# Kernel optimization log

Measured on AMD Instinct MI355X. Metric: run time of the kernel, lower is better.

Reference implementation:

```python
import jax, jax.numpy as jnp
import numpy as np

N = 50000   # nodes
E = 600000  # edges (avg degree 12)
F = 16      # raw node features
P = 32      # n_channels_preproc
C = 128     # n_channels
L = 6       # n_gnn_layers
LBL = 2     # n_labels


def _dense_init(k, fan_in, shape):
    return (jax.random.normal(k, shape, jnp.float32) / np.float32(np.sqrt(fan_in)))


def setup_inputs() -> dict:
    key = jax.random.key(0)
    ks = jax.random.split(key, 12)
    return {
        "x": jax.random.normal(ks[0], (N, F), jnp.float32),
        "edge_src": jax.random.randint(ks[1], (E,), 0, N, dtype=jnp.int32),
        "edge_dst": jax.random.randint(ks[2], (E,), 0, N, dtype=jnp.int32),
        "edge_weight": jax.random.uniform(ks[3], (E,), jnp.float32),  # normalized-adjacency values
        "preproc_W": _dense_init(ks[4], F, (F, P)), "preproc_b": jnp.zeros((P,), jnp.float32),
        "fc_in1_W": _dense_init(ks[5], P, (P, C)), "fc_in1_b": jnp.zeros((C,), jnp.float32),
        "fc_in2_W": _dense_init(ks[6], P, (P, C)), "fc_in2_b": jnp.zeros((C,), jnp.float32),
        "gcn_W": _dense_init(ks[7], C, (L, C, C)), "gcn_b": jnp.zeros((L, C), jnp.float32),
        "fcg_W": _dense_init(ks[8], 2 * C, (L, 2 * C, C)), "fcg_b": jnp.zeros((L, C), jnp.float32),
        "last1_W": _dense_init(ks[9], 2 * C, (2 * C, C)), "last1_b": jnp.zeros((C,), jnp.float32),
        "last2_W": _dense_init(ks[10], C, (C, LBL)), "last2_b": jnp.zeros((LBL,), jnp.float32),
    }


def reference(x, edge_src, edge_dst, edge_weight,
              preproc_W, preproc_b, fc_in1_W, fc_in1_b, fc_in2_W, fc_in2_b,
              gcn_W, gcn_b, fcg_W, fcg_b, last1_W, last1_b, last2_W, last2_b):
    relu = jax.nn.relu
    h = relu(x @ preproc_W + preproc_b)                      # preproc Dense
    node_id = relu(h @ fc_in1_W + fc_in1_b)                  # node identity branch
    h = relu(h @ fc_in2_W + fc_in2_b)

    def layer(h, params):
        W, b, Wf, bf = params
        # GCNConv: act(A_hat @ (h @ W) + b), A_hat as COO edge list
        hw = h @ W                                           # [N, C]
        msg = hw[edge_src] * edge_weight[:, None]            # [E, C]
        agg = jax.ops.segment_sum(msg, edge_dst, num_segments=N)
        g = relu(agg + b)
        merged = jnp.concatenate([node_id, g], axis=-1)      # [N, 2C]
        return relu(merged @ Wf + bf), None                  # dropout = identity (eval)

    h, _ = jax.lax.scan(layer, h, (gcn_W, gcn_b, fcg_W, fcg_b))

    merged = jnp.concatenate([node_id, h], axis=-1)
    h = relu(merged @ last1_W + last1_b)
    return jax.nn.sigmoid(h @ last2_W + last2_b)             # [N, n_labels]
```

## Files before the change

### kernel.cpp

```cpp
#include <hip/hip_runtime.h>
#include <cstddef>
#include <cstdint>

#define NN 50000
#define NE 600000
#define NB 391

typedef __attribute__((ext_vector_type(8))) short bf16x8;
typedef __attribute__((ext_vector_type(4))) float f32x4;

#define SWZ(x) (((x) ^ ((x) >> 2)) & 3)

__device__ __forceinline__ float bf2f(ushort u) {
    return __uint_as_float(((uint32_t)u) << 16);
}
__device__ __forceinline__ ushort f2bf(float f) {
    uint32_t b = __float_as_uint(f);
    return (ushort)((b + 0x7FFF + ((b >> 16) & 1)) >> 16);
}

__global__ __launch_bounds__(256)
void convbh_kernel(const float* __restrict__ f1W, const float* __restrict__ f2W,
                   const float* __restrict__ gW, const float* __restrict__ fgW,
                   const float* __restrict__ l1W, ushort* __restrict__ wt,
                   const int* __restrict__ dst, int* __restrict__ bcnt)
{
    if (blockIdx.x < 1312) {
        int i = blockIdx.x * 256 + threadIdx.x;
        if (i >= 335872) return;
        float v;
        if (i < 4096) {
            int c = i >> 5, k = i & 31;
            v = f1W[k * 128 + c];
        } else if (i < 8192) {
            int j = i - 4096; int c = j >> 5, k = j & 31;
            v = f2W[k * 128 + c];
        } else if (i < 8192 + 98304) {
            int j = i - 8192; int l = j >> 14, r = j & 16383;
            int c = r >> 7, k = r & 127;
            v = gW[l * 16384 + k * 128 + c];
        } else if (i < 8192 + 98304 + 196608) {
            int j = i - (8192 + 98304); int l = j >> 15, r = j & 32767;
            int c = r >> 8, k = r & 255;
            v = fgW[l * 32768 + k * 128 + c];
        } else {
            int j = i - (8192 + 98304 + 196608);
            int c = j >> 8, k = j & 255;
            v = l1W[k * 128 + c];
        }
        wt[i] = f2bf(v);
    } else {
        __shared__ int h[NB];
        int tx = threadIdx.x;
        for (int i = tx; i < NB; i += 256) h[i] = 0;
        __syncthreads();
        int e0 = (blockIdx.x - 1312) * 1024;
#pragma unroll
        for (int k = 0; k < 4; ++k) {
            int e = e0 + k * 256 + tx;
            if (e < NE) atomicAdd(&h[dst[e] >> 7], 1);
        }
        __syncthreads();
        for (int i = tx; i < NB; i += 256)
            if (h[i]) atomicAdd(&bcnt[i], h[i]);
    }
}

__global__ __launch_bounds__(512)
void bscan_kernel(const int* __restrict__ bcnt, int* __restrict__ bbase,
                  int* __restrict__ bcur)
{
    __shared__ int buf[512];
    int t = threadIdx.x;
    int v = (t < NB) ? bcnt[t] : 0;
    buf[t] = v;
    __syncthreads();
    for (int s = 1; s < 512; s <<= 1) {
        int u = (t >= s) ? buf[t - s] : 0;
        __syncthreads();
        buf[t] += u;
        __syncthreads();
    }
    if (t < NB) {
        int ex = buf[t] - v;
        bbase[t] = ex;
        bcur[t]  = ex;
    }
    if (t == 0) bbase[NB] = NE;
}

__global__ __launch_bounds__(256)
void pass1_kernel(const int* __restrict__ src, const int* __restrict__ dst,
                  const float* __restrict__ w, int* __restrict__ bcur,
                  unsigned int* __restrict__ stage_pk,
// ... 61 lines not shown
        int node0 = b * 128;
        if (tx < 128) {
            int n = node0 + tx;
            if (n < NN) off[n] = base + lofs[tx];
            h[tx] = 0;
        }
        if (b == NB - 1 && tx == 0) off[NN] = NE;
        __syncthreads();
        for (int i = tx; i < cnt; i += 256) {
            int d = stage_dl[base + i];
            int r = atomicAdd(&h[d], 1);
            esw[base + lofs[d] + r] = stage_pk[base + i];
        }
    } else {
        __shared__ float Wl[512];
        __shared__ float bl[32];
        int tx = threadIdx.x;
        Wl[tx]       = preW[tx];
        Wl[tx + 256] = preW[tx + 256];
        if (tx < 32) bl[tx] = preb[tx];
        __syncthreads();
        int n = (blockIdx.x - NB) * 256 + tx;
        if (n >= NN) return;
        float xr[16];
        const float4* xp = (const float4*)(x + (size_t)n * 16);
#pragma unroll
        for (int q = 0; q < 4; ++q) {
            float4 v = xp[q];
            xr[q*4+0]=v.x; xr[q*4+1]=v.y; xr[q*4+2]=v.z; xr[q*4+3]=v.w;
        }
        float acc[32];
#pragma unroll
        for (int c = 0; c < 32; ++c) acc[c] = bl[c];
#pragma unroll
        for (int k = 0; k < 16; ++k)
#pragma unroll
            for (int c = 0; c < 32; ++c)
                acc[c] = fmaf(xr[k], Wl[k*32+c], acc[c]);
        ushort4* op = (ushort4*)(h0b + (size_t)n * 32);
#pragma unroll
        for (int q = 0; q < 8; ++q) {
            ushort4 v;
            v.x = f2bf(fmaxf(acc[q*4+0], 0.f));
            v.y = f2bf(fmaxf(acc[q*4+1], 0.f));
            v.z = f2bf(fmaxf(acc[q*4+2], 0.f));
            v.w = f2bf(fmaxf(acc[q*4+3], 0.f));
            op[q] = v;
        }
    }
}

__global__ __launch_bounds__(128)
void fc1f0_kernel(const ushort* __restrict__ h0b,
                  const ushort* __restrict__ wf1, const float* __restrict__ f1b,
                  ushort* __restrict__ nidb,
                  const ushort* __restrict__ wf2, const float* __restrict__ f2b,
                  const ushort* __restrict__ wg, ushort* __restrict__ hwb)
{
    __shared__ ushort Atile[64 * 32];
    __shared__ ushort Btile[128 * 32];
    __shared__ ushort Xt[64 * 128];
    const int tx   = threadIdx.x;
    const int wave = tx >> 6;
    const int lane = tx & 63;
    const int rs  = lane >> 2;
    const int chn = (lane & 3) ^ SWZ(rs);
    const int m    = lane & 15;
    const int quad = lane >> 4;
    const int slot = quad ^ SWZ(m);

    if (blockIdx.x < 782) {
        const int bm = blockIdx.x * 64;
        f32x4 acc0[8], acc1[8];
#pragma unroll
        for (int t = 0; t < 8; ++t) {
            acc0[t] = (f32x4){0.f, 0.f, 0.f, 0.f};
            acc1[t] = (f32x4){0.f, 0.f, 0.f, 0.f};
        }
#pragma unroll
        for (int i = 0; i < 2; ++i) {
            int seg = wave + 2 * i;
            int row = seg * 16 + rs;
            int ar  = bm + row; if (ar >= NN) ar = NN - 1;
            __builtin_amdgcn_global_load_lds(
                (const __attribute__((address_space(1))) void*)
                    (h0b + (size_t)ar * 32 + chn * 8),
                (__attribute__((address_space(3))) void*)(Atile + seg * 512),
                16, 0, 0);
        }
#pragma unroll
        for (int i = 0; i < 4; ++i) {
            int seg = wave + 2 * i;
            int col = seg * 16 + rs;
            __builtin_amdgcn_global_load_lds(
                (const __attribute__((address_space(1))) void*)
                    (wf1 + (size_t)col * 32 + chn * 8),
                (__attribute__((address_space(3))) void*)(Btile + seg * 512),
                16, 0, 0);
        }
        __syncthreads();
        bf16x8 af0 = *(const bf16x8*)(Atile + (wave * 32 + m) * 32 + slot * 8);
        bf16x8 af1 = *(const bf16x8*)(Atile + (wave * 32 + 16 + m) * 32 + slot * 8);
#pragma unroll
        for (int t = 0; t < 8; ++t) {
            bf16x8 bfr = *(const bf16x8*)(Btile + (t * 16 + m) * 32 + slot * 8);
            acc0[t] = __builtin_amdgcn_mfma_f32_16x16x32_bf16(af0, bfr, acc0[t], 0, 0, 0);
            acc1[t] = __builtin_amdgcn_mfma_f32_16x16x32_bf16(af1, bfr, acc1[t], 0, 0, 0);
        }
        __syncthreads();
#pragma unroll
        for (int half = 0; half < 2; ++half) {
            const int orow0 = bm + wave * 32 + half * 16 + quad * 4;
#pragma unroll
            for (int t = 0; t < 8; ++t) {
                int col = t * 16 + m;
                float bb = f1b[col];
                f32x4 a = half ? acc1[t] : acc0[t];
#pragma unroll
                for (int r = 0; r < 4; ++r) {
                    int row = orow0 + r;
                    if (row < NN)
                        nidb[(size_t)row * 128 + col] = f2bf(fmaxf(a[r] + bb, 0.f));
                }
            }
        }
    } else {
        const int bm = (blockIdx.x - 782) * 64;
        f32x4 acc0[8], acc1[8];
#pragma unroll
        for (int t = 0; t < 8; ++t) {
            acc0[t] = (f32x4){0.f, 0.f, 0.f, 0.f};
            acc1[t] = (f32x4){0.f, 0.f, 0.f, 0.f};
        }
#pragma unroll
        for (int i = 0; i < 2; ++i) {
            int seg = wave + 2 * i;
            int row = seg * 16 + rs;
            int ar  = bm + row; if (ar >= NN) ar = NN - 1;
            __builtin_amdgcn_global_load_lds(
                (const __attribute__((address_space(1))) void*)
                    (h0b + (size_t)ar * 32 + chn * 8),
                (__attribute__((address_space(3))) void*)(Atile + seg * 512),
                16, 0, 0);
        }
#pragma unroll
        for (int i = 0; i < 4; ++i) {
            int seg = wave + 2 * i;
            int col = seg * 16 + rs;
            __builtin_amdgcn_global_load_lds(
                (const __attribute__((address_space(1))) void*)
                    (wf2 + (size_t)col * 32 + chn * 8),
                (__attribute__((address_space(3))) void*)(Btile + seg * 512),
                16, 0, 0);
        }
        __syncthreads();
        {
            bf16x8 af0 = *(const bf16x8*)(Atile + (wave * 32 + m) * 32 + slot * 8);
            bf16x8 af1 = *(const bf16x8*)(Atile + (wave * 32 + 16 + m) * 32 + slot * 8);
#pragma unroll
            for (int t = 0; t < 8; ++t) {
                bf16x8 bfr = *(const bf16x8*)(Btile + (t * 16 + m) * 32 + slot * 8);
                acc0[t] = __builtin_amdgcn_mfma_f32_16x16x32_bf16(af0, bfr, acc0[t], 0, 0, 0);
                acc1[t] = __builtin_amdgcn_mfma_f32_16x16x32_bf16(af1, bfr, acc1[t], 0, 0, 0);
            }
        }
        __syncthreads();
#pragma unroll
        for (int half = 0; half < 2; ++half) {
            int rbase = wave * 32 + half * 16 + quad * 4;
#pragma unroll
            for (int t = 0; t < 8; ++t) {
                int col = t * 16 + m;
                float bb = f2b[col];
                int c32 = col >> 5, within = col & 7, ks = (col >> 3) & 3;
                f32x4 a = half ? acc1[t] : acc0[t];
#pragma unroll
                for (int r = 0; r < 4; ++r) {
                    int row = rbase + r;
                    int pos = ks ^ SWZ(row & 15);
                    Xt[row * 128 + c32 * 32 + pos * 8 + within] =
                        f2bf(fmaxf(a[r] + bb, 0.f));
                }
            }
        }
#pragma unroll
        for (int t = 0; t < 8; ++t) {
            acc0[t] = (f32x4){0.f, 0.f, 0.f, 0.f};
            acc1[t] = (f32x4){0.f, 0.f, 0.f, 0.f};
        }
        __syncthreads();
        for (int c32 = 0; c32 < 4; ++c32) {
            int kk = c32 * 32;
#pragma unroll
            for (int i = 0; i < 4; ++i) {
                int seg = wave + 2 * i;
                int col = seg * 16 + rs;
                __builtin_amdgcn_global_load_lds(
                    (const __attribute__((address_space(1))) void*)
                        (wg + (size_t)col * 128 + kk + chn * 8),
                    (__attribute__((address_space(3))) void*)(Btile + seg * 512),
                    16, 0, 0);
            }
            __syncthreads();
            bf16x8 af0 = *(const bf16x8*)(Xt + (wave * 32 + m) * 128 + kk + slot * 8);
            bf16x8 af1 = *(const bf16x8*)(Xt + (wave * 32 + 16 + m) * 128 + kk + slot * 8);
#pragma unroll
            for (int t = 0; t < 8; ++t) {
                bf16x8 bfr = *(const bf16x8*)(Btile + (t * 16 + m) * 32 + slot * 8);
                acc0[t] = __builtin_amdgcn_mfma_f32_16x16x32_bf16(af0, bfr, acc0[t], 0, 0, 0);
                acc1[t] = __builtin_amdgcn_mfma_f32_16x16x32_bf16(af1, bfr, acc1[t], 0, 0, 0);
            }
            __syncthreads();
        }
#pragma unroll
        for (int half = 0; half < 2; ++half) {
            const int orow0 = bm + wave * 32 + half * 16 + quad * 4;
#pragma unroll
            for (int t = 0; t < 8; ++t) {
                int col = t * 16 + m;
                f32x4 a = half ? acc1[t] : acc0[t];
#pragma unroll
                for (int r = 0; r < 4; ++r) {
                    int row = orow0 + r;
                    if (row < NN)
                        hwb[(size_t)row * 128 + col] = f2bf(a[r]);
                }
            }
        }
    }
}

__global__ __launch_bounds__(128)
void gemm_fused(const ushort* __restrict__ A1, int K1,
                const ushort* __restrict__ A2, int K2,
                const ushort* __restrict__ Wt, const float* __restrict__ bias,
                const ushort* __restrict__ Wg,
                ushort* __restrict__ out_hw, int nrows)
{
    __shared__ ushort Atile[64 * 32];
    __shared__ ushort Btile[128 * 32];
    __shared__ ushort Xt[64 * 128];
    const int tx   = threadIdx.x;
    const int wave = tx >> 6;
    const int lane = tx & 63;
    const int bm   = blockIdx.x * 64;
    const int Ktot = K1 + K2;

    const int rs  = lane >> 2;
    const int chn = (lane & 3) ^ SWZ(rs);
    const int m    = lane & 15;
    const int quad = lane >> 4;
    const int slot = quad ^ SWZ(m);

    f32x4 acc0[8], acc1[8];
#pragma unroll
    for (int t = 0; t < 8; ++t) {
        acc0[t] = (f32x4){0.f, 0.f, 0.f, 0.f};
        acc1[t] = (f32x4){0.f, 0.f, 0.f, 0.f};
    }

    for (int kk = 0; kk < Ktot; kk += 32) {
        const ushort* asrc; int astr, kl;
        if (kk < K1) { asrc = A1; astr = K1; kl = kk; }
        else         { asrc = A2; astr = K2; kl = kk - K1; }
#pragma unroll
        for (int i = 0; i < 2; ++i) {
            int seg = wave + 2 * i;
            int row = seg * 16 + rs;
            int ar  = bm + row; if (ar >= nrows) ar = nrows - 1;
            __builtin_amdgcn_global_load_lds(
                (const __attribute__((address_space(1))) void*)
                    (asrc + (size_t)ar * astr + kl + chn * 8),
                (__attribute__((address_space(3))) void*)(Atile + seg * 512),
                16, 0, 0);
        }
#pragma unroll
        for (int i = 0; i < 4; ++i) {
            int seg = wave + 2 * i;
            int col = seg * 16 + rs;
            __builtin_amdgcn_global_load_lds(
                (const __attribute__((address_space(1))) void*)
                    (Wt + (size_t)col * Ktot + kk + chn * 8),
                (__attribute__((address_space(3))) void*)(Btile + seg * 512),
                16, 0, 0);
        }
        __syncthreads();
        bf16x8 af0 = *(const bf16x8*)(Atile + (wave * 32 + m) * 32 + slot * 8);
        bf16x8 af1 = *(const bf16x8*)(Atile + (wave * 32 + 16 + m) * 32 + slot * 8);
#pragma unroll
        for (int t = 0; t < 8; ++t) {
            bf16x8 bfr = *(const bf16x8*)(Btile + (t * 16 + m) * 32 + slot * 8);
            acc0[t] = __builtin_amdgcn_mfma_f32_16x16x32_bf16(af0, bfr, acc0[t], 0, 0, 0);
            acc1[t] = __builtin_amdgcn_mfma_f32_16x16x32_bf16(af1, bfr, acc1[t], 0, 0, 0);
        }
        __syncthreads();
    }

#pragma unroll
    for (int half = 0; half < 2; ++half) {
        int rbase = wave * 32 + half * 16 + quad * 4;
#pragma unroll
        for (int t = 0; t < 8; ++t) {
            int col = t * 16 + m;
            float bb = bias[col];
            int c32 = col >> 5, within = col & 7, ks = (col >> 3) & 3;
            f32x4 a = half ? acc1[t] : acc0[t];
#pragma unroll
            for (int r = 0; r < 4; ++r) {
                int row = rbase + r;
                int pos = ks ^ SWZ(row & 15);
                Xt[row * 128 + c32 * 32 + pos * 8 + within] =
                    f2bf(fmaxf(a[r] + bb, 0.f));
            }
        }
    }
#pragma unroll
    for (int t = 0; t < 8; ++t) {
        acc0[t] = (f32x4){0.f, 0.f, 0.f, 0.f};
        acc1[t] = (f32x4){0.f, 0.f, 0.f, 0.f};
    }
    __syncthreads();

    for (int c32 = 0; c32 < 4; ++c32) {
        int kk = c32 * 32;
#pragma unroll
        for (int i = 0; i < 4; ++i) {
            int seg = wave + 2 * i;
            int col = seg * 16 + rs;
            __builtin_amdgcn_global_load_lds(
                (const __attribute__((address_space(1))) void*)
                    (Wg + (size_t)col * 128 + kk + chn * 8),
                (__attribute__((address_space(3))) void*)(Btile + seg * 512),
                16, 0, 0);
        }
        __syncthreads();
        bf16x8 af0 = *(const bf16x8*)(Xt + (wave * 32 + m) * 128 + kk + slot * 8);
        bf16x8 af1 = *(const bf16x8*)(Xt + (wave * 32 + 16 + m) * 128 + kk + slot * 8);
#pragma unroll
        for (int t = 0; t < 8; ++t) {
            bf16x8 bfr = *(const bf16x8*)(Btile + (t * 16 + m) * 32 + slot * 8);
            acc0[t] = __builtin_amdgcn_mfma_f32_16x16x32_bf16(af0, bfr, acc0[t], 0, 0, 0);
            acc1[t] = __builtin_amdgcn_mfma_f32_16x16x32_bf16(af1, bfr, acc1[t], 0, 0, 0);
        }
        __syncthreads();
    }

#pragma unroll
    for (int half = 0; half < 2; ++half) {
        const int orow0 = bm + wave * 32 + half * 16 + quad * 4;
#pragma unroll
        for (int t = 0; t < 8; ++t) {
            int col = t * 16 + m;
            f32x4 a = half ? acc1[t] : acc0[t];
#pragma unroll
            for (int r = 0; r < 4; ++r) {
                int row = orow0 + r;
                if (row < nrows)
                    out_hw[(size_t)row * 128 + col] = f2bf(a[r]);
            }
        }
    }
}

__global__ __launch_bounds__(128)
void gemm_last(const ushort* __restrict__ nid, const ushort* __restrict__ agg,
               const ushort* __restrict__ Wt, const float* __restrict__ bias5,
               const ushort* __restrict__ Wl1, const float* __restrict__ l1b,
               const float* __restrict__ l2W, const float* __restrict__ l2b,
               float* __restrict__ out, int nrows)
{
    __shared__ ushort Atile[64 * 32];
    __shared__ ushort Btile[128 * 32];
    __shared__ ushort Xt[64 * 128];
    __shared__ float  w2s[256];
    const int tx   = threadIdx.x;
    const int wave = tx >> 6;
    const int lane = tx & 63;
    const int bm   = blockIdx.x * 64;

    w2s[tx]       = l2W[tx];
    w2s[tx + 128] = l2W[tx + 128];

    const int rs  = lane >> 2;
    const int chn = (lane & 3) ^ SWZ(rs);
    const int m    = lane & 15;
    const int quad = lane >> 4;
    const int slot = quad ^ SWZ(m);

    f32x4 acc0[8], acc1[8];
#pragma unroll
    for (int t = 0; t < 8; ++t) {
        acc0[t] = (f32x4){0.f, 0.f, 0.f, 0.f};
        acc1[t] = (f32x4){0.f, 0.f, 0.f, 0.f};
    }

    for (int kk = 0; kk < 256; kk += 32) {
        const ushort* asrc; int kl;
        if (kk < 128) { asrc = nid; kl = kk; }
        else          { asrc = agg; kl = kk - 128; }
#pragma unroll
        for (int i = 0; i < 2; ++i) {
            int seg = wave + 2 * i;
            int row = seg * 16 + rs;
            int ar  = bm + row; if (ar >= nrows) ar = nrows - 1;
            __builtin_amdgcn_global_load_lds(
                (const __attribute__((address_space(1))) void*)
                    (asrc + (size_t)ar * 128 + kl + chn * 8),
                (__attribute__((address_space(3))) void*)(Atile + seg * 512),
                16, 0, 0);
        }
#pragma unroll
        for (int i = 0; i < 4; ++i) {
            int seg = wave + 2 * i;
            int col = seg * 16 + rs;
            __builtin_amdgcn_global_load_lds(
                (const __attribute__((address_space(1))) void*)
                    (Wt + (size_t)col * 256 + kk + chn * 8),
                (__attribute__((address_space(3))) void*)(Btile + seg * 512),
                16, 0, 0);
        }
        __syncthreads();
        bf16x8 af0 = *(const bf16x8*)(Atile + (wave * 32 + m) * 32 + slot * 8);
        bf16x8 af1 = *(const bf16x8*)(Atile + (wave * 32 + 16 + m) * 32 + slot * 8);
#pragma unroll
        for (int t = 0; t < 8; ++t) {
            bf16x8 bfr = *(const bf16x8*)(Btile + (t * 16 + m) * 32 + slot * 8);
            acc0[t] = __builtin_amdgcn_mfma_f32_16x16x32_bf16(af0, bfr, acc0[t], 0, 0, 0);
            acc1[t] = __builtin_amdgcn_mfma_f32_16x16x32_bf16(af1, bfr, acc1[t], 0, 0, 0);
        }
        __syncthreads();
    }

#pragma unroll
    for (int half = 0; half < 2; ++half) {
        int rbase = wave * 32 + half * 16 + quad * 4;
#pragma unroll
        for (int t = 0; t < 8; ++t) {
            int col = t * 16 + m;
            float bb = bias5[col];
            int c32 = col >> 5, within = col & 7, ks = (col >> 3) & 3;
            f32x4 a = half ? acc1[t] : acc0[t];
#pragma unroll
            for (int r = 0; r < 4; ++r) {
                int row = rbase + r;
                int pos = ks ^ SWZ(row & 15);
                Xt[row * 128 + c32 * 32 + pos * 8 + within] =
                    f2bf(fmaxf(a[r] + bb, 0.f));
            }
        }
    }
#pragma unroll
    for (int t = 0; t < 8; ++t) {
        acc0[t] = (f32x4){0.f, 0.f, 0.f, 0.f};
        acc1[t] = (f32x4){0.f, 0.f, 0.f, 0.f};
    }
    __syncthreads();

    for (int c8 = 0; c8 < 8; ++c8) {
        int kk = c8 * 32;
        if (c8 < 4) {
#pragma unroll
            for (int i = 0; i < 2; ++i) {
                int seg = wave + 2 * i;
                int row = seg * 16 + rs;
                int ar  = bm + row; if (ar >= nrows) ar = nrows - 1;
                __builtin_amdgcn_global_load_lds(
                    (const __attribute__((address_space(1))) void*)
                        (nid + (size_t)ar * 128 + kk + chn * 8),
                    (__attribute__((address_space(3))) void*)(Atile + seg * 512),
                    16, 0, 0);
            }
        }
#pragma unroll
        for (int i = 0; i < 4; ++i) {
            int seg = wave + 2 * i;
            int col = seg * 16 + rs;
            __builtin_amdgcn_global_load_lds(
                (const __attribute__((address_space(1))) void*)
                    (Wl1 + (size_t)col * 256 + kk + chn * 8),
                (__attribute__((address_space(3))) void*)(Btile + seg * 512),
                16, 0, 0);
        }
        __syncthreads();
        bf16x8 af0, af1;
        if (c8 < 4) {
            af0 = *(const bf16x8*)(Atile + (wave * 32 + m) * 32 + slot * 8);
            af1 = *(const bf16x8*)(Atile + (wave * 32 + 16 + m) * 32 + slot * 8);
        } else {
            int ko = (c8 - 4) * 32;
            af0 = *(const bf16x8*)(Xt + (wave * 32 + m) * 128 + ko + slot * 8);
            af1 = *(const bf16x8*)(Xt + (wave * 32 + 16 + m) * 128 + ko + slot * 8);
        }
#pragma unroll
        for (int t = 0; t < 8; ++t) {
            bf16x8 bfr = *(const bf16x8*)(Btile + (t * 16 + m) * 32 + slot * 8);
            acc0[t] = __builtin_amdgcn_mfma_f32_16x16x32_bf16(af0, bfr, acc0[t], 0, 0, 0);
            acc1[t] = __builtin_amdgcn_mfma_f32_16x16x32_bf16(af1, bfr, acc1[t], 0, 0, 0);
        }
        __syncthreads();
    }

    float bb[8];
#pragma unroll
    for (int t = 0; t < 8; ++t) bb[t] = l1b[t * 16 + m];
    float b20 = l2b[0], b21 = l2b[1];
#pragma unroll
    for (int half = 0; half < 2; ++half) {
#pragma unroll
        for (int r = 0; r < 4; ++r) {
            float p0 = 0.f, p1 = 0.f;
#pragma unroll
            for (int t = 0; t < 8; ++t) {
                int col = t * 16 + m;
                f32x4 a = half ? acc1[t] : acc0[t];
                float v = fmaxf(a[r] + bb[t], 0.f);
                p0 = fmaf(v, w2s[col * 2 + 0], p0);
                p1 = fmaf(v, w2s[col * 2 + 1], p1);
            }
#pragma unroll
            for (int mask = 1; mask < 16; mask <<= 1) {
                p0 += __shfl_xor(p0, mask);
                p1 += __shfl_xor(p1, mask);
            }
            if (m == 0) {
                int row = bm + wave * 32 + half * 16 + quad * 4 + r;
                if (row < nrows) {
                    out[(size_t)row * 2 + 0] = 1.f / (1.f + __expf(-(p0 + b20)));
                    out[(size_t)row * 2 + 1] = 1.f / (1.f + __expf(-(p1 + b21)));
                }
            }
        }
    }
}

__global__ __launch_bounds__(256)
void gather_agg(const ushort* __restrict__ hw,
                const unsigned int* __restrict__ esw,
                const int* __restrict__ off, const float* __restrict__ gbias,
                ushort* __restrict__ agg)
{
    const int g    = blockIdx.x * 4 + (threadIdx.x >> 6);
    const int lane = threadIdx.x & 63;
    int n = g * 8;
    if (n >= NN) return;
    int n_end = n + 8; if (n_end > NN) n_end = NN;
    const int base = off[n];
    const int end  = off[n_end];
    int nb = off[n + 1];
    const ushort* hp = hw + lane * 2;
    const float g0 = gbias[lane * 2], g1 = gbias[lane * 2 + 1];
    float a0 = 0.f, a1 = 0.f;

    for (int chunk = base; chunk < end; chunk += 64) {
        int idx = chunk + lane;
        int pk = (idx < end) ? (int)esw[idx] : 0;
        int cnt = end - chunk; if (cnt > 64) cnt = 64;
        int cnt16 = (cnt + 15) & ~15;
        for (int j = 0; j < cnt16; j += 16) {
            int pp[16];
            unsigned int rv[16];
#pragma unroll
            for (int k = 0; k < 16; ++k)
                pp[k] = __builtin_amdgcn_readlane(pk, j + k);
#pragma unroll
            for (int k = 0; k < 16; ++k)
                rv[k] = *(const unsigned int*)(hp + (size_t)(pp[k] & 0x1FFFF) * 128);
#pragma unroll
            for (int k = 0; k < 16; ++k) {
                int e = chunk + j + k;
                while (e == nb) {
                    unsigned int o = (unsigned int)f2bf(fmaxf(a0 + g0, 0.f)) |
                                     ((unsigned int)f2bf(fmaxf(a1 + g1, 0.f)) << 16);
                    *(unsigned int*)(agg + (size_t)n * 128 + lane * 2) = o;
                    a0 = 0.f; a1 = 0.f;
                    ++n;
                    nb = (n < n_end) ? off[n + 1] : 0x7fffffff;
                }
                float w = bf2f((ushort)((unsigned int)pp[k] >> 17));
                a0 = fmaf(bf2f((ushort)(rv[k] & 0xffff)), w, a0);
                a1 = fmaf(bf2f((ushort)(rv[k] >> 16)),    w, a1);
            }
        }
    }
    while (n < n_end) {
        unsigned int o = (unsigned int)f2bf(fmaxf(a0 + g0, 0.f)) |
                         ((unsigned int)f2bf(fmaxf(a1 + g1, 0.f)) << 16);
        *(unsigned int*)(agg + (size_t)n * 128 + lane * 2) = o;
        a0 = 0.f; a1 = 0.f;
        ++n;
    }
}

extern "C" void kernel_launch(void* const* d_in, const int* in_sizes, int n_in,
                              void* d_out, int out_size, void* d_ws, size_t ws_size,
                              hipStream_t stream)
{
    const float* x    = (const float*)d_in[0];
    const int*   esrc = (const int*)  d_in[1];
    const int*   edst = (const int*)  d_in[2];
    const float* ew   = (const float*)d_in[3];
    const float* preW = (const float*)d_in[4];
    const float* preb = (const float*)d_in[5];
    const float* f1W  = (const float*)d_in[6];
    const float* f1b  = (const float*)d_in[7];
    const float* f2W  = (const float*)d_in[8];
    const float* f2b  = (const float*)d_in[9];
    const float* gW   = (const float*)d_in[10];
    const float* gb   = (const float*)d_in[11];
    const float* fgW  = (const float*)d_in[12];
    const float* fgb  = (const float*)d_in[13];
    const float* l1W  = (const float*)d_in[14];
    const float* l1b  = (const float*)d_in[15];
    const float* l2W  = (const float*)d_in[16];
    const float* l2b  = (const float*)d_in[17];
    float* out = (float*)d_out;

    ushort* wt   = (ushort*)d_ws;
    ushort* wf1  = wt;
    ushort* wf2  = wf1 + 4096;
    ushort* wg   = wf2 + 4096;
    ushort* wfg  = wg  + 98304;
    ushort* wl1  = wfg + 196608;
    ushort* h0b  = wl1 + 32768;
    ushort* nidb = h0b  + (size_t)NN * 32;
    ushort* hwb  = nidb + (size_t)NN * 128;
    ushort* aggb = hwb  + (size_t)NN * 128;
    ushort* endu = aggb + (size_t)NN * 128;
    unsigned int* esw      = (unsigned int*)(((uintptr_t)endu + 15) & ~(uintptr_t)15);
    unsigned int* stage_pk = esw + NE;
    int*          bcnt     = (int*)(stage_pk + NE);
    int*          bbase    = bcnt + NB + 1;
    int*          bcur     = bbase + NB + 1;
    int*          off      = bcur + NB + 1;
    unsigned char* stage_dl = (unsigned char*)(off + NN + 2);

    const int gblocks = (NN + 63) / 64;
    const int eblocks = (NE + 1023) / 1024;
    const int ngroups = (NN + 7) / 8;
    const int wblocks = (ngroups + 3) / 4;

    hipMemsetAsync(bcnt, 0, (size_t)NB * sizeof(int), stream);
    convbh_kernel<<<1312 + eblocks, 256, 0, stream>>>(f1W, f2W, gW, fgW, l1W, wt,
                                                      edst, bcnt);
    bscan_kernel<<<1, 512, 0, stream>>>(bcnt, bbase, bcur);
    pass1_kernel<<<eblocks, 256, 0, stream>>>(esrc, edst, ew, bcur, stage_pk, stage_dl);
    p2pre_kernel<<<NB + (NN + 255) / 256, 256, 0, stream>>>(stage_pk, stage_dl, bbase,
                                                            esw, off, x, preW, preb, h0b);

    fc1f0_kernel<<<2 * gblocks, 128, 0, stream>>>(h0b, wf1, f1b, nidb,
                                                  wf2, f2b, wg, hwb);
    for (int l = 0; l < 6; ++l) {
        gather_agg<<<wblocks, 256, 0, stream>>>(hwb, esw, off,
                                                gb + (size_t)l * 128, aggb);
        if (l < 5) {
            gemm_fused<<<gblocks, 128, 0, stream>>>(nidb, 128, aggb, 128,
                                                    wfg + (size_t)l * 32768,
                                                    fgb + (size_t)l * 128,
                                                    wg + (size_t)(l + 1) * 16384,
                                                    hwb, NN);
        }
    }
    gemm_last<<<gblocks, 128, 0, stream>>>(nidb, aggb,
                                           wfg + (size_t)5 * 32768,
                                           fgb + (size_t)5 * 128,
                                           wl1, l1b, l2W, l2b, out, NN);
}
```

Measured before the change: 420.4 us.

## Fuse edge gather-aggregation into per-layer GEMM kernels with ping-pong hw buffers

Removes the separate gather_agg kernel and performs the CSR gather/segment-sum for each 64-row tile directly inside the layer GEMM kernel. The aggregated rows are written into a swizzled LDS tile instead of a global agg buffer. Blocks grow to 4 waves with 16 rows each, and hw is double-buffered so one layer can read hw while the next layer's hw is written. This drops six kernel launches and the global write and re-read of the agg tensor. In exchange, LDS use per block rises and the gather and MFMA phases are serialized inside each block, which may reduce occupancy.

Measured after the change: 508.7 us. +21.0%, slower.

```diff
diff --git a/kernel.cpp b/kernel.cpp
--- a/kernel.cpp
+++ b/kernel.cpp
@@ -10,6 +10,11 @@
 typedef __attribute__((ext_vector_type(4))) float f32x4;
 
 #define SWZ(x) (((x) ^ ((x) >> 2)) & 3)
+
+#define GLDS16(src, dst)                                                     \
+    __builtin_amdgcn_global_load_lds(                                        \
+        (const __attribute__((address_space(1))) void*)(src),                \
+        (__attribute__((address_space(3))) void*)(dst), 16, 0, 0)
 
 __device__ __forceinline__ float bf2f(ushort u) {
     return __uint_as_float(((uint32_t)u) << 16);
@@ -237,21 +242,13 @@
             int seg = wave + 2 * i;
             int row = seg * 16 + rs;
             int ar  = bm + row; if (ar >= NN) ar = NN - 1;
-            __builtin_amdgcn_global_load_lds(
-                (const __attribute__((address_space(1))) void*)
-                    (h0b + (size_t)ar * 32 + chn * 8),
-                (__attribute__((address_space(3))) void*)(Atile + seg * 512),
-                16, 0, 0);
+            GLDS16(h0b + (size_t)ar * 32 + chn * 8, Atile + seg * 512);
         }
 #pragma unroll
         for (int i = 0; i < 4; ++i) {
             int seg = wave + 2 * i;
             int col = seg * 16 + rs;
-            __builtin_amdgcn_global_load_lds(
-                (const __attribute__((address_space(1))) void*)
-                    (wf1 + (size_t)col * 32 + chn * 8),
-                (__attribute__((address_space(3))) void*)(Btile + seg * 512),
-                16, 0, 0);
+            GLDS16(wf1 + (size_t)col * 32 + chn * 8, Btile + seg * 512);
         }
         __syncthreads();
         bf16x8 af0 = *(const bf16x8*)(Atile + (wave * 32 + m) * 32 + slot * 8);
@@ -292,21 +289,13 @@
             int seg = wave + 2 * i;
             int row = seg * 16 + rs;
             int ar  = bm + row; if (ar >= NN) ar = NN - 1;
-            __builtin_amdgcn_global_load_lds(
-                (const __attribute__((address_space(1))) void*)
-                    (h0b + (size_t)ar * 32 + chn * 8),
-                (__attribute__((address_space(3))) void*)(Atile + seg * 512),
-                16, 0, 0);
+            GLDS16(h0b + (size_t)ar * 32 + chn * 8, Atile + seg * 512);
         }
 #pragma unroll
         for (int i = 0; i < 4; ++i) {
             int seg = wave + 2 * i;
             int col = seg * 16 + rs;
-            __builtin_amdgcn_global_load_lds(
-                (const __attribute__((address_space(1))) void*)
-                    (wf2 + (size_t)col * 32 + chn * 8),
-                (__attribute__((address_space(3))) void*)(Btile + seg * 512),
-                16, 0, 0);
+            GLDS16(wf2 + (size_t)col * 32 + chn * 8, Btile + seg * 512);
         }
         __syncthreads();
         {
@@ -350,11 +339,7 @@
             for (int i = 0; i < 4; ++i) {
                 int seg = wave + 2 * i;
                 int col = seg * 16 + rs;
-                __builtin_amdgcn_global_load_lds(
-                    (const __attribute__((address_space(1))) void*)
-                        (wg + (size_t)col * 128 + kk + chn * 8),
-                    (__attribute__((address_space(3))) void*)(Btile + seg * 512),
-                    16, 0, 0);
+                GLDS16(wg + (size_t)col * 128 + kk + chn * 8, Btile + seg * 512);
             }
             __syncthreads();
             bf16x8 af0 = *(const bf16x8*)(Xt + (wave * 32 + m) * 128 + kk + slot * 8);
@@ -385,140 +370,197 @@
     }
 }
 
-__global__ __launch_bounds__(128)
-void gemm_fused(const ushort* __restrict__ A1, int K1,
-                const ushort* __restrict__ A2, int K2,
-                const ushort* __restrict__ Wt, const float* __restrict__ bias,
-                const ushort* __restrict__ Wg,
-                ushort* __restrict__ out_hw, int nrows)
+__global__ __launch_bounds__(256)
+void gemm_gather(const ushort* __restrict__ hw,
+                 const unsigned int* __restrict__ esw,
+                 const int* __restrict__ off,
+                 const float* __restrict__ gbias,
+                 const ushort* __restrict__ nid,
+                 const ushort* __restrict__ Wt,
+                 const float* __restrict__ bias,
+                 const ushort* __restrict__ Wg,
+                 ushort* __restrict__ out_hw, int nrows)
 {
     __shared__ ushort Atile[64 * 32];
     __shared__ ushort Btile[128 * 32];
     __shared__ ushort Xt[64 * 128];
+    __shared__ ushort Agg[64 * 128];
     const int tx   = threadIdx.x;
     const int wave = tx >> 6;
     const int lane = tx & 63;
     const int bm   = blockIdx.x * 64;
-    const int Ktot = K1 + K2;
-
-    const int rs  = lane >> 2;
-    const int chn = (lane & 3) ^ SWZ(rs);
+    const int rs   = lane >> 2;
+    const int chn  = (lane & 3) ^ SWZ(rs);
     const int m    = lane & 15;
     const int quad = lane >> 4;
     const int slot = quad ^ SWZ(m);
 
-    f32x4 acc0[8], acc1[8];
-#pragma unroll
-    for (int t = 0; t < 8; ++t) {
-        acc0[t] = (f32x4){0.f, 0.f, 0.f, 0.f};
-        acc1[t] = (f32x4){0.f, 0.f, 0.f, 0.f};
-    }
-
-    for (int kk = 0; kk < Ktot; kk += 32) {
-        const ushort* asrc; int astr, kl;
-        if (kk < K1) { asrc = A1; astr = K1; kl = kk; }
-        else         { asrc = A2; astr = K2; kl = kk - K1; }
+    {
+        int ar = bm + wave * 16 + rs; if (ar >= nrows) ar = nrows - 1;
+        GLDS16(nid + (size_t)ar * 128 + chn * 8, Atile + wave * 512);
 #pragma unroll
         for (int i = 0; i < 2; ++i) {
-            int seg = wave + 2 * i;
-            int row = seg * 16 + rs;
-            int ar  = bm + row; if (ar >= nrows) ar = nrows - 1;
-            __builtin_amdgcn_global_load_lds(
-                (const __attribute__((address_space(1))) void*)
-                    (asrc + (size_t)ar * astr + kl + chn * 8),
-                (__attribute__((address_space(3))) void*)(Atile + seg * 512),
-                16, 0, 0);
-        }
-#pragma unroll
-        for (int i = 0; i < 4; ++i) {
-            int seg = wave + 2 * i;
+            int seg = wave + 4 * i;
             int col = seg * 16 + rs;
-            __builtin_amdgcn_global_load_lds(
-                (const __attribute__((address_space(1))) void*)
-                    (Wt + (size_t)col * Ktot + kk + chn * 8),
-                (__attribute__((address_space(3))) void*)(Btile + seg * 512),
-                16, 0, 0);
-        }
-        __syncthreads();
-        bf16x8 af0 = *(const bf16x8*)(Atile + (wave * 32 + m) * 32 + slot * 8);
-        bf16x8 af1 = *(const bf16x8*)(Atile + (wave * 32 + 16 + m) * 32 + slot * 8);
+            GLDS16(Wt + (size_t)col * 256 + chn * 8, Btile + seg * 512);
+        }
+    }
+
+    {
+        const int n0   = bm + wave * 16;
+        const int nend = n0 + 16;
+        int n    = n0;
+        const int base = off[n0 < NN ? n0 : NN];
+        const int end  = off[nend < NN ? nend : NN];
+        int nb = (n < NN) ? off[n + 1] : 0x7fffffff;
+        const ushort* hp = hw + lane * 2;
+        const float g0 = gbias[lane * 2], g1 = gbias[lane * 2 + 1];
+        float a0 = 0.f, a1 = 0.f;
+        const int c32g = lane >> 4;
+        const int ksg  = (lane >> 2) & 3;
+        const int wth  = (2 * lane) & 7;
+        for (int chunk = base; chunk < end; chunk += 64) {
+            int idx = chunk + lane;
+            int pk = (idx < end) ? (int)esw[idx] : 0;
+            int cnt = end - chunk; if (cnt > 64) cnt = 64;
+            int cnt16 = (cnt + 15) & ~15;
+            for (int j = 0; j < cnt16; j += 16) {
+                int pp[16];
+                unsigned int rv[16];
+#pragma unroll
+                for (int k = 0; k < 16; ++k)
+                    pp[k] = __builtin_amdgcn_readlane(pk, j + k);
+#pragma unroll
+                for (int k = 0; k < 16; ++k)
+                    rv[k] = *(const unsigned int*)(hp + (size_t)(pp[k] & 0x1FFFF) * 128);
+#pragma unroll
+                for (int k = 0; k < 16; ++k) {
+                    int e = chunk + j + k;
+                    while (e == nb) {
+                        int row = n - bm;
+                        unsigned int o = (unsigned int)f2bf(fmaxf(a0 + g0, 0.f)) |
+                                         ((unsigned int)f2bf(fmaxf(a1 + g1, 0.f)) << 16);
+                        int pos = ksg ^ SWZ(row & 15);
+                        *(unsigned int*)(Agg + row * 128 + c32g * 32 + pos * 8 + wth) = o;
+                        a0 = 0.f; a1 = 0.f;
+                        ++n;
+                        nb = (n < nend && n < NN) ? off[n + 1] : 0x7fffffff;
+                    }
+                    float w = bf2f((ushort)((unsigned int)pp[k] >> 17));
+                    a0 = fmaf(bf2f((ushort)(rv[k] & 0xffff)), w, a0);
+                    a1 = fmaf(bf2f((ushort)(rv[k] >> 16)),    w, a1);
+                }
+            }
+        }
+        while (n < nend) {
+            int row = n - bm;
+            unsigned int o = (unsigned int)f2bf(fmaxf(a0 + g0, 0.f)) |
+                             ((unsigned int)f2bf(fmaxf(a1 + g1, 0.f)) << 16);
+            int pos = ksg ^ SWZ(row & 15);
+            *(unsigned int*)(Agg + row * 128 + c32g * 32 + pos * 8 + wth) = o;
+            a0 = 0.f; a1 = 0.f;
+            ++n;
+        }
+    }
+
+    f32x4 acc[8];
+#pragma unroll
+    for (int t = 0; t < 8; ++t) acc[t] = (f32x4){0.f, 0.f, 0.f, 0.f};
+
+    for (int c8 = 0; c8 < 8; ++c8) {
+        int kk = c8 * 32;
+        if (c8 > 0) {
+            if (c8 < 4) {
+                int ar = bm + wave * 16 + rs; if (ar >= nrows) ar = nrows - 1;
+                GLDS16(nid + (size_t)ar * 128 + kk + chn * 8, Atile + wave * 512);
+            }
+#pragma unroll
+            for (int i = 0; i < 2; ++i) {
+                int seg = wave + 4 * i;
+                int col = seg * 16 + rs;
+                GLDS16(Wt + (size_t)col * 256 + kk + chn * 8, Btile + seg * 512);
+            }
+        }
+        __syncthreads();
+        bf16x8 af = (c8 < 4)
+            ? *(const bf16x8*)(Atile + (wave * 16 + m) * 32 + slot * 8)
+            : *(const bf16x8*)(Agg + (wave * 16 + m) * 128 + (kk - 128) + slot * 8);
 #pragma unroll
         for (int t = 0; t < 8; ++t) {
             bf16x8 bfr = *(const bf16x8*)(Btile + (t * 16 + m) * 32 + slot * 8);
-            acc0[t] = __builtin_amdgcn_mfma_f32_16x16x32_bf16(af0, bfr, acc0[t], 0, 0, 0);
-            acc1[t] = __builtin_amdgcn_mfma_f32_16x16x32_bf16(af1, bfr, acc1[t], 0, 0, 0);
-        }
-        __syncthreads();
-    }
-
-#pragma unroll
-    for (int half = 0; half < 2; ++half) {
-        int rbase = wave * 32 + half * 16 + quad * 4;
+            acc[t] = __builtin_amdgcn_mfma_f32_16x16x32_bf16(af, bfr, acc[t], 0, 0, 0);
+        }
+        __syncthreads();
+    }
+
+#pragma unroll
+    for (int i = 0; i < 2; ++i) {
+        int seg = wave + 4 * i;
+        int col = seg * 16 + rs;
+        GLDS16(Wg + (size_t)col * 128 + chn * 8, Btile + seg * 512);
+    }
+
+    {
+        int rbase = wave * 16 + quad * 4;
 #pragma unroll
         for (int t = 0; t < 8; ++t) {
             int col = t * 16 + m;
             float bb = bias[col];
             int c32 = col >> 5, within = col & 7, ks = (col >> 3) & 3;
-            f32x4 a = half ? acc1[t] : acc0[t];
 #pragma unroll
             for (int r = 0; r < 4; ++r) {
                 int row = rbase + r;
                 int pos = ks ^ SWZ(row & 15);
                 Xt[row * 128 + c32 * 32 + pos * 8 + within] =
-                    f2bf(fmaxf(a[r] + bb, 0.f));
-            }
-        }
-    }
-#pragma unroll
-    for (int t = 0; t < 8; ++t) {
-        acc0[t] = (f32x4){0.f, 0.f, 0.f, 0.f};
-        acc1[t] = (f32x4){0.f, 0.f, 0.f, 0.f};
-    }
+                    f2bf(fmaxf(acc[t][r] + bb, 0.f));
+            }
+        }
+    }
+#pragma unroll
+    for (int t = 0; t < 8; ++t) acc[t] = (f32x4){0.f, 0.f, 0.f, 0.f};
     __syncthreads();
 
-    for (int c32 = 0; c32 < 4; ++c32) {
-        int kk = c32 * 32;
-#pragma unroll
-        for (int i = 0; i < 4; ++i) {
-            int seg = wave + 2 * i;
-            int col = seg * 16 + rs;
-            __builtin_amdgcn_global_load_lds(
-                (const __attribute__((address_space(1))) void*)
-                    (Wg + (size_t)col * 128 + kk + chn * 8),
-                (__attribute__((address_space(3))) void*)(Btile + seg * 512),
-                16, 0, 0);
-        }
-        __syncthreads();
-        bf16x8 af0 = *(const bf16x8*)(Xt + (wave * 32 + m) * 128 + kk + slot * 8);
-        bf16x8 af1 = *(const bf16x8*)(Xt + (wave * 32 + 16 + m) * 128 + kk + slot * 8);
+    for (int c4 = 0; c4 < 4; ++c4) {
+        int kk = c4 * 32;
+        if (c4 > 0) {
+#pragma unroll
+            for (int i = 0; i < 2; ++i) {
+                int seg = wave + 4 * i;
+                int col = seg * 16 + rs;
+                GLDS16(Wg + (size_t)col * 128 + kk + chn * 8, Btile + seg * 512);
+            }
+        }
+        __syncthreads();
+        bf16x8 af = *(const bf16x8*)(Xt + (wave * 16 + m) * 128 + kk + slot * 8);
 #pragma unroll
         for (int t = 0; t < 8; ++t) {
             bf16x8 bfr = *(const bf16x8*)(Btile + (t * 16 + m) * 32 + slot * 8);
-            acc0[t] = __builtin_amdgcn_mfma_f32_16x16x32_bf16(af0, bfr, acc0[t], 0, 0, 0);
-            acc1[t] = __builtin_amdgcn_mfma_f32_16x16x32_bf16(af1, bfr, acc1[t], 0, 0, 0);
-        }
-        __syncthreads();
-    }
-
-#pragma unroll
-    for (int half = 0; half < 2; ++half) {
-        const int orow0 = bm + wave * 32 + half * 16 + quad * 4;
+            acc[t] = __builtin_amdgcn_mfma_f32_16x16x32_bf16(af, bfr, acc[t], 0, 0, 0);
+        }
+        __syncthreads();
+    }
+
+    {
+        const int orow0 = bm + wave * 16 + quad * 4;
 #pragma unroll
         for (int t = 0; t < 8; ++t) {
             int col = t * 16 + m;
-            f32x4 a = half ? acc1[t] : acc0[t];
 #pragma unroll
             for (int r = 0; r < 4; ++r) {
                 int row = orow0 + r;
                 if (row < nrows)
-                    out_hw[(size_t)row * 128 + col] = f2bf(a[r]);
-            }
-        }
-    }
-}
-
-__global__ __launch_bounds__(128)
-void gemm_last(const ushort* __restrict__ nid, const ushort* __restrict__ agg,
+                    out_hw[(size_t)row * 128 + col] = f2bf(acc[t][r]);
+            }
+        }
+    }
+}
+
+__global__ __launch_bounds__(256)
+void gemm_last(const ushort* __restrict__ hw,
+               const unsigned int* __restrict__ esw,
+               const int* __restrict__ off,
+               const float* __restrict__ gbias,
+               const ushort* __restrict__ nid,
                const ushort* __restrict__ Wt, const float* __restrict__ bias5,
                const ushort* __restrict__ Wl1, const float* __restrict__ l1b,
                const float* __restrict__ l2W, const float* __restrict__ l2b,
@@ -527,130 +569,175 @@
     __shared__ ushort Atile[64 * 32];
     __shared__ ushort Btile[128 * 32];
     __shared__ ushort Xt[64 * 128];
+    __shared__ ushort Agg[64 * 128];
     __shared__ float  w2s[256];
     const int tx   = threadIdx.x;
     const int wave = tx >> 6;
     const int lane = tx & 63;
     const int bm   = blockIdx.x * 64;
-
-    w2s[tx]       = l2W[tx];
-    w2s[tx + 128] = l2W[tx + 128];
-
-    const int rs  = lane >> 2;
-    const int chn = (lane & 3) ^ SWZ(rs);
+    const int rs   = lane >> 2;
+    const int chn  = (lane & 3) ^ SWZ(rs);
     const int m    = lane & 15;
     const int quad = lane >> 4;
     const int slot = quad ^ SWZ(m);
 
-    f32x4 acc0[8], acc1[8];
-#pragma unroll
-    for (int t = 0; t < 8; ++t) {
-        acc0[t] = (f32x4){0.f, 0.f, 0.f, 0.f};
-        acc1[t] = (f32x4){0.f, 0.f, 0.f, 0.f};
-    }
-
-    for (int kk = 0; kk < 256; kk += 32) {
-        const ushort* asrc; int kl;
-        if (kk < 128) { asrc = nid; kl = kk; }
-        else          { asrc = agg; kl = kk - 128; }
+    w2s[tx] = l2W[tx];
+
+    {
+        int ar = bm + wave * 16 + rs; if (ar >= nrows) ar = nrows - 1;
+        GLDS16(nid + (size_t)ar * 128 + chn * 8, Atile + wave * 512);
 #pragma unroll
         for (int i = 0; i < 2; ++i) {
-            int seg = wave + 2 * i;
-            int row = seg * 16 + rs;
-            int ar  = bm + row; if (ar >= nrows) ar = nrows - 1;
-            __builtin_amdgcn_global_load_lds(
-                (const __attribute__((address_space(1))) void*)
-                    (asrc + (size_t)ar * 128 + kl + chn * 8),
-                (__attribute__((address_space(3))) void*)(Atile + seg * 512),
-                16, 0, 0);
-        }
-#pragma unroll
-        for (int i = 0; i < 4; ++i) {
-            int seg = wave + 2 * i;
+            int seg = wave + 4 * i;
             int col = seg * 16 + rs;
-            __builtin_amdgcn_global_load_lds(
-                (const __attribute__((address_space(1))) void*)
-                    (Wt + (size_t)col * 256 + kk + chn * 8),
-                (__attribute__((address_space(3))) void*)(Btile + seg * 512),
-                16, 0, 0);
-        }
-        __syncthreads();
-        bf16x8 af0 = *(const bf16x8*)(Atile + (wave * 32 + m) * 32 + slot * 8);
-        bf16x8 af1 = *(const bf16x8*)(Atile + (wave * 32 + 16 + m) * 32 + slot * 8);
+            GLDS16(Wt + (size_t)col * 256 + chn * 8, Btile + seg * 512);
+        }
+    }
+
+    {
+        const int n0   = bm + wave * 16;
+        const int nend = n0 + 16;
+        int n    = n0;
+        const int base = off[n0 < NN ? n0 : NN];
+        const int end  = off[nend < NN ? nend : NN];
+        int nb = (n < NN) ? off[n + 1] : 0x7fffffff;
+        const ushort* hp = hw + lane * 2;
+        const float g0 = gbias[lane * 2], g1 = gbias[lane * 2 + 1];
+        float a0 = 0.f, a1 = 0.f;
+        const int c32g = lane >> 4;
+        const int ksg  = (lane >> 2) & 3;
+        const int wth  = (2 * lane) & 7;
+        for (int chunk = base; chunk < end; chunk += 64) {
+            int idx = chunk + lane;
+            int pk = (idx < end) ? (int)esw[idx] : 0;
+            int cnt = end - chunk; if (cnt > 64) cnt = 64;
+            int cnt16 = (cnt + 15) & ~15;
+            for (int j = 0; j < cnt16; j += 16) {
+                int pp[16];
+                unsigned int rv[16];
+#pragma unroll
+                for (int k = 0; k < 16; ++k)
+                    pp[k] = __builtin_amdgcn_readlane(pk, j + k);
+#pragma unroll
+                for (int k = 0; k < 16; ++k)
+                    rv[k] = *(const unsigned int*)(hp + (size_t)(pp[k] & 0x1FFFF) * 128);
+#pragma unroll
+                for (int k = 0; k < 16; ++k) {
+                    int e = chunk + j + k;
+                    while (e == nb) {
+                        int row = n - bm;
+                        unsigned int o = (unsigned int)f2bf(fmaxf(a0 + g0, 0.f)) |
+                                         ((unsigned int)f2bf(fmaxf(a1 + g1, 0.f)) << 16);
+                        int pos = ksg ^ SWZ(row & 15);
+                        *(unsigned int*)(Agg + row * 128 + c32g * 32 + pos * 8 + wth) = o;
+                        a0 = 0.f; a1 = 0.f;
+                        ++n;
+                        nb = (n < nend && n < NN) ? off[n + 1] : 0x7fffffff;
+                    }
+                    float w = bf2f((ushort)((unsigned int)pp[k] >> 17));
+                    a0 = fmaf(bf2f((ushort)(rv[k] & 0xffff)), w, a0);
+                    a1 = fmaf(bf2f((ushort)(rv[k] >> 16)),    w, a1);
+                }
+            }
+        }
+        while (n < nend) {
+            int row = n - bm;
+            unsigned int o = (unsigned int)f2bf(fmaxf(a0 + g0, 0.f)) |
+                             ((unsigned int)f2bf(fmaxf(a1 + g1, 0.f)) << 16);
+            int pos = ksg ^ SWZ(row & 15);
+            *(unsigned int*)(Agg + row * 128 + c32g * 32 + pos * 8 + wth) = o;
+            a0 = 0.f; a1 = 0.f;
+            ++n;
+        }
+    }
+
+    f32x4 acc[8];
+#pragma unroll
+    for (int t = 0; t < 8; ++t) acc[t] = (f32x4){0.f, 0.f, 0.f, 0.f};
+
+    for (int c8 = 0; c8 < 8; ++c8) {
+        int kk = c8 * 32;
+        if (c8 > 0) {
+            if (c8 < 4) {
+                int ar = bm + wave * 16 + rs; if (ar >= nrows) ar = nrows - 1;
+                GLDS16(nid + (size_t)ar * 128 + kk + chn * 8, Atile + wave * 512);
+            }
+#pragma unroll
+            for (int i = 0; i < 2; ++i) {
+                int seg = wave + 4 * i;
+                int col = seg * 16 + rs;
+                GLDS16(Wt + (size_t)col * 256 + kk + chn * 8, Btile + seg * 512);
+            }
+        }
+        __syncthreads();
+        bf16x8 af = (c8 < 4)
+            ? *(const bf16x8*)(Atile + (wave * 16 + m) * 32 + slot * 8)
+            : *(const bf16x8*)(Agg + (wave * 16 + m) * 128 + (kk - 128) + slot * 8);
 #pragma unroll
         for (int t = 0; t < 8; ++t) {
             bf16x8 bfr = *(const bf16x8*)(Btile + (t * 16 + m) * 32 + slot * 8);
-            acc0[t] = __builtin_amdgcn_mfma_f32_16x16x32_bf16(af0, bfr, acc0[t], 0, 0, 0);
-            acc1[t] = __builtin_amdgcn_mfma_f32_16x16x32_bf16(af1, bfr, acc1[t], 0, 0, 0);
-        }
-        __syncthreads();
-    }
-
-#pragma unroll
-    for (int half = 0; half < 2; ++half) {
-        int rbase = wave * 32 + half * 16 + quad * 4;
+            acc[t] = __builtin_amdgcn_mfma_f32_16x16x32_bf16(af, bfr, acc[t], 0, 0, 0);
+        }
+        __syncthreads();
+    }
+
+    {
+        int ar = bm + wave * 16 + rs; if (ar >= nrows) ar = nrows - 1;
+        GLDS16(nid + (size_t)ar * 128 + chn * 8, Atile + wave * 512);
+#pragma unroll
+        for (int i = 0; i < 2; ++i) {
+            int seg = wave + 4 * i;
+            int col = seg * 16 + rs;
+            GLDS16(Wl1 + (size_t)col * 256 + chn * 8, Btile + seg * 512);
+        }
+    }
+
+    {
+        int rbase = wave * 16 + quad * 4;
 #pragma unroll
         for (int t = 0; t < 8; ++t) {
             int col = t * 16 + m;
             float bb = bias5[col];
             int c32 = col >> 5, within = col & 7, ks = (col >> 3) & 3;
-            f32x4 a = half ? acc1[t] : acc0[t];
 #pragma unroll
             for (int r = 0; r < 4; ++r) {
                 int row = rbase + r;
                 int pos = ks ^ SWZ(row & 15);
                 Xt[row * 128 + c32 * 32 + pos * 8 + within] =
-                    f2bf(fmaxf(a[r] + bb, 0.f));
-            }
-        }
-    }
-#pragma unroll
-    for (int t = 0; t < 8; ++t) {
-        acc0[t] = (f32x4){0.f, 0.f, 0.f, 0.f};
-        acc1[t] = (f32x4){0.f, 0.f, 0.f, 0.f};
-    }
+                    f2bf(fmaxf(acc[t][r] + bb, 0.f));
+            }
+        }
+    }
+#pragma unroll
+    for (int t = 0; t < 8; ++t) acc[t] = (f32x4){0.f, 0.f, 0.f, 0.f};
     __syncthreads();
 
     for (int c8 = 0; c8 < 8; ++c8) {
         int kk = c8 * 32;
+        if (c8 > 0) {
+            if (c8 < 4) {
+                int ar = bm + wave * 16 + rs; if (ar >= nrows) ar = nrows - 1;
+                GLDS16(nid + (size_t)ar * 128 + kk + chn * 8, Atile + wave * 512);
+            }
+#pragma unroll
+            for (int i = 0; i < 2; ++i) {
+                int seg = wave + 4 * i;
+                int col = seg * 16 + rs;
+                GLDS16(Wl1 + (size_t)col * 256 + kk + chn * 8, Btile + seg * 512);
+            }
+        }
+        __syncthreads();
+        bf16x8 af;
         if (c8 < 4) {
-#pragma unroll
-            for (int i = 0; i < 2; ++i) {
-                int seg = wave + 2 * i;
-                int row = seg * 16 + rs;
-                int ar  = bm + row; if (ar >= nrows) ar = nrows - 1;
-                __builtin_amdgcn_global_load_lds(
-                    (const __attribute__((address_space(1))) void*)
-                        (nid + (size_t)ar * 128 + kk + chn * 8),
-                    (__attribute__((address_space(3))) void*)(Atile + seg * 512),
-                    16, 0, 0);
-            }
-        }
-#pragma unroll
-        for (int i = 0; i < 4; ++i) {
-            int seg = wave + 2 * i;
-            int col = seg * 16 + rs;
-            __builtin_amdgcn_global_load_lds(
-                (const __attribute__((address_space(1))) void*)
-                    (Wl1 + (size_t)col * 256 + kk + chn * 8),
-                (__attribute__((address_space(3))) void*)(Btile + seg * 512),
-                16, 0, 0);
-        }
-        __syncthreads();
-        bf16x8 af0, af1;
-        if (c8 < 4) {
-            af0 = *(const bf16x8*)(Atile + (wave * 32 + m) * 32 + slot * 8);
-            af1 = *(const bf16x8*)(Atile + (wave * 32 + 16 + m) * 32 + slot * 8);
+            af = *(const bf16x8*)(Atile + (wave * 16 + m) * 32 + slot * 8);
         } else {
             int ko = (c8 - 4) * 32;
-            af0 = *(const bf16x8*)(Xt + (wave * 32 + m) * 128 + ko + slot * 8);
-            af1 = *(const bf16x8*)(Xt + (wave * 32 + 16 + m) * 128 + ko + slot * 8);
+            af = *(const bf16x8*)(Xt + (wave * 16 + m) * 128 + ko + slot * 8);
         }
 #pragma unroll
         for (int t = 0; t < 8; ++t) {
             bf16x8 bfr = *(const bf16x8*)(Btile + (t * 16 + m) * 32 + slot * 8);
-            acc0[t] = __builtin_amdgcn_mfma_f32_16x16x32_bf16(af0, bfr, acc0[t], 0, 0, 0);
-            acc1[t] = __builtin_amdgcn_mfma_f32_16x16x32_bf16(af1, bfr, acc1[t], 0, 0, 0);
+            acc[t] = __builtin_amdgcn_mfma_f32_16x16x32_bf16(af, bfr, acc[t], 0, 0, 0);
         }
         __syncthreads();
     }
@@ -660,89 +747,27 @@
     for (int t = 0; t < 8; ++t) bb[t] = l1b[t * 16 + m];
     float b20 = l2b[0], b21 = l2b[1];
 #pragma unroll
-    for (int half = 0; half < 2; ++half) {
-#pragma unroll
-        for (int r = 0; r < 4; ++r) {
-            float p0 = 0.f, p1 = 0.f;
-#pragma unroll
-            for (int t = 0; t < 8; ++t) {
-                int col = t * 16 + m;
-                f32x4 a = half ? acc1[t] : acc0[t];
-                float v = fmaxf(a[r] + bb[t], 0.f);
-                p0 = fmaf(v, w2s[col * 2 + 0], p0);
-                p1 = fmaf(v, w2s[col * 2 + 1], p1);
-            }
-#pragma unroll
-            for (int mask = 1; mask < 16; mask <<= 1) {
-                p0 += __shfl_xor(p0, mask);
-                p1 += __shfl_xor(p1, mask);
-            }
-            if (m == 0) {
-                int row = bm + wave * 32 + half * 16 + quad * 4 + r;
-                if (row < nrows) {
-                    out[(size_t)row * 2 + 0] = 1.f / (1.f + __expf(-(p0 + b20)));
-                    out[(size_t)row * 2 + 1] = 1.f / (1.f + __expf(-(p1 + b21)));
-                }
-            }
-        }
-    }
-}
-
-__global__ __launch_bounds__(256)
-void gather_agg(const ushort* __restrict__ hw,
-                const unsigned int* __restrict__ esw,
-                const int* __restrict__ off, const float* __restrict__ gbias,
-                ushort* __restrict__ agg)
-{
-    const int g    = blockIdx.x * 4 + (threadIdx.x >> 6);
-    const int lane = threadIdx.x & 63;
-    int n = g * 8;
-    if (n >= NN) return;
-    int n_end = n + 8; if (n_end > NN) n_end = NN;
-    const int base = off[n];
-    const int end  = off[n_end];
-    int nb = off[n + 1];
-    const ushort* hp = hw + lane * 2;
-    const float g0 = gbias[lane * 2], g1 = gbias[lane * 2 + 1];
-    float a0 = 0.f, a1 = 0.f;
-
-    for (int chunk = base; chunk < end; chunk += 64) {
-        int idx = chunk + lane;
-        int pk = (idx < end) ? (int)esw[idx] : 0;
-        int cnt = end - chunk; if (cnt > 64) cnt = 64;
-        int cnt16 = (cnt + 15) & ~15;
-        for (int j = 0; j < cnt16; j += 16) {
-            int pp[16];
-            unsigned int rv[16];
-#pragma unroll
-            for (int k = 0; k < 16; ++k)
-                pp[k] = __builtin_amdgcn_readlane(pk, j + k);
-#pragma unroll
-            for (int k = 0; k < 16; ++k)
-                rv[k] = *(const unsigned int*)(hp + (size_t)(pp[k] & 0x1FFFF) * 128);
-#pragma unroll
-            for (int k = 0; k < 16; ++k) {
-                int e = chunk + j + k;
-                while (e == nb) {
-                    unsigned int o = (unsigned int)f2bf(fmaxf(a0 + g0, 0.f)) |
-                                     ((unsigned int)f2bf(fmaxf(a1 + g1, 0.f)) << 16);
-                    *(unsigned int*)(agg + (size_t)n * 128 + lane * 2) = o;
-                    a0 = 0.f; a1 = 0.f;
-                    ++n;
-                    nb = (n < n_end) ? off[n + 1] : 0x7fffffff;
-                }
-                float w = bf2f((ushort)((unsigned int)pp[k] >> 17));
-                a0 = fmaf(bf2f((ushort)(rv[k] & 0xffff)), w, a0);
-                a1 = fmaf(bf2f((ushort)(rv[k] >> 16)),    w, a1);
-            }
-        }
-    }
-    while (n < n_end) {
-        unsigned int o = (unsigned int)f2bf(fmaxf(a0 + g0, 0.f)) |
-                         ((unsigned int)f2bf(fmaxf(a1 + g1, 0.f)) << 16);
-        *(unsigned int*)(agg + (size_t)n * 128 + lane * 2) = o;
-        a0 = 0.f; a1 = 0.f;
-        ++n;
+    for (int r = 0; r < 4; ++r) {
+        float p0 = 0.f, p1 = 0.f;
+#pragma unroll
+        for (int t = 0; t < 8; ++t) {
+            int col = t * 16 + m;
+            float v = fmaxf(acc[t][r] + bb[t], 0.f);
+            p0 = fmaf(v, w2s[col * 2 + 0], p0);
+            p1 = fmaf(v, w2s[col * 2 + 1], p1);
+        }
+#pragma unroll
+        for (int mask = 1; mask < 16; mask <<= 1) {
+            p0 += __shfl_xor(p0, mask);
+            p1 += __shfl_xor(p1, mask);
+        }
+        if (m == 0) {
+            int row = bm + wave * 16 + quad * 4 + r;
+            if (row < nrows) {
+                out[(size_t)row * 2 + 0] = 1.f / (1.f + __expf(-(p0 + b20)));
+                out[(size_t)row * 2 + 1] = 1.f / (1.f + __expf(-(p1 + b21)));
+            }
+        }
     }
 }
 
@@ -779,8 +804,8 @@
     ushort* h0b  = wl1 + 32768;
     ushort* nidb = h0b  + (size_t)NN * 32;
     ushort* hwb  = nidb + (size_t)NN * 128;
-    ushort* aggb = hwb  + (size_t)NN * 128;
-    ushort* endu = aggb + (size_t)NN * 128;
+    ushort* hwb2 = hwb  + (size_t)NN * 128;
+    ushort* endu = hwb2 + (size_t)NN * 128;
     unsigned int* esw      = (unsigned int*)(((uintptr_t)endu + 15) & ~(uintptr_t)15);
     unsigned int* stage_pk = esw + NE;
     int*          bcnt     = (int*)(stage_pk + NE);
@@ -791,8 +816,6 @@
 
     const int gblocks = (NN + 63) / 64;
     const int eblocks = (NE + 1023) / 1024;
-    const int ngroups = (NN + 7) / 8;
-    const int wblocks = (ngroups + 3) / 4;
 
     hipMemsetAsync(bcnt, 0, (size_t)NB * sizeof(int), stream);
     convbh_kernel<<<1312 + eblocks, 256, 0, stream>>>(f1W, f2W, gW, fgW, l1W, wt,
@@ -804,18 +827,19 @@
 
     fc1f0_kernel<<<2 * gblocks, 128, 0, stream>>>(h0b, wf1, f1b, nidb,
                                                   wf2, f2b, wg, hwb);
-    for (int l = 0; l < 6; ++l) {
-        gather_agg<<<wblocks, 256, 0, stream>>>(hwb, esw, off,
-                                                gb + (size_t)l * 128, aggb);
-        if (l < 5) {
-            gemm_fused<<<gblocks, 128, 0, stream>>>(nidb, 128, aggb, 128,
-                                                    wfg + (size_t)l * 32768,
-                                                    fgb + (size_t)l * 128,
-                                                    wg + (size_t)(l + 1) * 16384,
-                                                    hwb, NN);
-        }
-    }
-    gemm_last<<<gblocks, 128, 0, stream>>>(nidb, aggb,
+    ushort* cur = hwb;
+    ushort* nxt = hwb2;
+    for (int l = 0; l < 5; ++l) {
+        gemm_gather<<<gblocks, 256, 0, stream>>>(cur, esw, off,
+                                                 gb + (size_t)l * 128, nidb,
+                                                 wfg + (size_t)l * 32768,
+                                                 fgb + (size_t)l * 128,
+                                                 wg + (size_t)(l + 1) * 16384,
+                                                 nxt, NN);
+        ushort* tmp = cur; cur = nxt; nxt = tmp;
+    }
+    gemm_last<<<gblocks, 256, 0, stream>>>(cur, esw, off,
+                                           gb + (size_t)5 * 128, nidb,
                                            wfg + (size_t)5 * 32768,
                                            fgb + (size_t)5 * 128,
                                            wl1, l1b, l2W, l2b, out, NN);
```
